# Optimization experiments

Measured on AMD Instinct MI355X. Metric: run time of the kernel, lower is better.

The kernel has to match this reference:

```python
import math
import jax, jax.numpy as jnp
import numpy as np

# ---- config (matches init_kwargs) ----
HIDDEN = 2048
N_HEADS = 16
Q_LORA = 1536
KV_LORA = 512
NOPE = 128
ROPE = 64
VHD = 128
QHD = NOPE + ROPE  # 192
BASE = 10000.0
SCALE = 40.0
ORIG_MAX = 4096
BETA_FAST = 32
BETA_SLOW = 1
MSCALE = 1.0
MSCALE_ALL = 1.0
EPS = 1e-6


def yarn_get_mscale(scale=1.0, mscale=1.0):
    if scale <= 1:
        return 1.0
    return 0.1 * mscale * math.log(scale) + 1.0


def yarn_cos_sin(seq_len):
    dim = ROPE
    ar = np.arange(0, dim, 2, dtype=np.float32)
    freq_extra = 1.0 / BASE ** (ar / dim)
    freq_inter = 1.0 / (SCALE * BASE ** (ar / dim))
    low = math.floor(dim * math.log(ORIG_MAX / (BETA_FAST * 2 * math.pi)) / (2 * math.log(BASE)))
    high = math.ceil(dim * math.log(ORIG_MAX / (BETA_SLOW * 2 * math.pi)) / (2 * math.log(BASE)))
    low, high = max(low, 0), min(high, dim - 1)
    denom = (high - low) if high != low else 0.001
    ramp = np.clip((np.arange(dim // 2, dtype=np.float32) - low) / denom, 0.0, 1.0)
    inv_freq_mask = 1.0 - ramp
    inv_freq = freq_inter * (1.0 - inv_freq_mask) + freq_extra * inv_freq_mask
    t = np.arange(seq_len, dtype=np.float32)
    freqs = np.outer(t, inv_freq)
    emb = np.concatenate([freqs, freqs], axis=-1)
    _m = yarn_get_mscale(SCALE, MSCALE) / yarn_get_mscale(SCALE, MSCALE_ALL)
    return jnp.asarray(np.cos(emb) * _m), jnp.asarray(np.sin(emb) * _m)


def rms_norm(x, w, eps=EPS):
    xf = x.astype(jnp.float32)
    var = jnp.mean(xf * xf, axis=-1, keepdims=True)
    return (w * (xf * jax.lax.rsqrt(var + eps)).astype(x.dtype))


def _rotate_half(x):
    x1, x2 = jnp.split(x, 2, axis=-1)
    return jnp.concatenate([-x2, x1], axis=-1)


def _interleave_to_half(x):
    # view(b,h,s,d//2,2).transpose(4,3).reshape(b,h,s,d)
    b, h, s, d = x.shape
    return jnp.swapaxes(x.reshape(b, h, s, d // 2, 2), -1, -2).reshape(b, h, s, d)


def apply_rope(q, k, cos, sin, position_ids):
    cos = cos[position_ids][:, None]  # [b,1,s,d]
    sin = sin[position_ids][:, None]
    q = _interleave_to_half(q)
    k = _interleave_to_half(k)
    q_emb = q * cos + _rotate_half(q) * sin
    k_emb = k * cos + _rotate_half(k) * sin
    return q_emb, k_emb


def mla_forward(hidden_states, position_ids, wq_a, q_a_ln_w, wq_b, wkv_a, kv_a_ln_w, wkv_b, wo):
    b, s, _ = hidden_states.shape
    # Q: low-rank down, RMSNorm, up
    q = rms_norm(hidden_states @ wq_a.T, q_a_ln_w) @ wq_b.T        # [b,s,H*QHD]
    q = q.reshape(b, s, N_HEADS, QHD).transpose(0, 2, 1, 3)        # [b,H,s,QHD]
    q_nope, q_pe = q[..., :NOPE], q[..., NOPE:]
    # KV: compressed latent + shared rope key
    ckv = hidden_states @ wkv_a.T                                   # [b,s,KV_LORA+ROPE]
    compressed, k_pe = ckv[..., :KV_LORA], ckv[..., KV_LORA:]
    k_pe = k_pe.reshape(b, s, 1, ROPE).transpose(0, 2, 1, 3)       # [b,1,s,ROPE]
    kv = rms_norm(compressed, kv_a_ln_w) @ wkv_b.T                  # [b,s,H*(NOPE+VHD)]
    kv = kv.reshape(b, s, N_HEADS, NOPE + VHD).transpose(0, 2, 1, 3)
    k_nope, value_states = kv[..., :NOPE], kv[..., NOPE:]
    # decoupled RoPE on rope dims only
    cos, sin = yarn_cos_sin(s)
    q_pe, k_pe = apply_rope(q_pe, k_pe, cos, sin, position_ids)
    query = jnp.concatenate([q_nope, q_pe], axis=-1)                # [b,H,s,QHD]
    key = jnp.concatenate(
        [k_nope, jnp.broadcast_to(k_pe, (b, N_HEADS, s, ROPE))], axis=-1)
    # softmax scale with YaRN mscale correction
    softmax_scale = QHD ** -0.5
    if MSCALE_ALL:
        m = yarn_get_mscale(SCALE, MSCALE_ALL)
        softmax_scale = softmax_scale * m * m
    attn = jnp.einsum('bhqd,bhkd->bhqk', query, key) * softmax_scale
    causal = jnp.tril(jnp.ones((s, s), dtype=bool))
    attn = jnp.where(causal, attn, jnp.finfo(attn.dtype).min)
    attn = jax.nn.softmax(attn.astype(jnp.float32), axis=-1).astype(query.dtype)
    out = jnp.einsum('bhqk,bhkd->bhqd', attn, value_states)         # [b,H,s,VHD]
    out = out.transpose(0, 2, 1, 3).reshape(b, s, N_HEADS * VHD)
    return out @ wo.T


def setup_inputs() -> dict:
    key = jax.random.key(0)
    ks = jax.random.split(key, 8)
    b, s = 2, 2048
    std = 0.02
    return {
        'hidden_states': jax.random.normal(ks[0], (b, s, HIDDEN), jnp.float32),
        'position_ids': jnp.broadcast_to(jnp.arange(s, dtype=jnp.int32), (b, s)),
        'wq_a': jax.random.normal(ks[1], (Q_LORA, HIDDEN), jnp.float32) * std,
        'q_a_ln_w': jnp.ones((Q_LORA,), jnp.float32),
        'wq_b': jax.random.normal(ks[2], (N_HEADS * QHD, Q_LORA), jnp.float32) * std,
        'wkv_a': jax.random.normal(ks[3], (KV_LORA + ROPE, HIDDEN), jnp.float32) * std,
        'kv_a_ln_w': jnp.ones((KV_LORA,), jnp.float32),
        'wkv_b': jax.random.normal(ks[4], (N_HEADS * (NOPE + VHD), KV_LORA), jnp.float32) * std,
        'wo': jax.random.normal(ks[5], (HIDDEN, N_HEADS * VHD), jnp.float32) * std,
    }


def reference(hidden_states, position_ids, wq_a, q_a_ln_w, wq_b, wkv_a, kv_a_ln_w, wkv_b, wo):
    return mla_forward(hidden_states, position_ids, wq_a, q_a_ln_w, wq_b,
                       wkv_a, kv_a_ln_w, wkv_b, wo)
```

## Files before the change

### kernel.cpp

```cpp
#include <hip/hip_runtime.h>
#include <hip/hip_bf16.h>
#include <math.h>

typedef __bf16 bf16_t;
typedef __bf16 bf16x4 __attribute__((ext_vector_type(4)));
typedef __bf16 bf16x8 __attribute__((ext_vector_type(8)));
typedef float floatx4 __attribute__((ext_vector_type(4)));

#define MFMA16(a, b, c) __builtin_amdgcn_mfma_f32_16x16x32_bf16((a), (b), (c), 0, 0, 0)

#define NEG_BIG (-1e30f)

__device__ __forceinline__ void gload16(const bf16_t* g, bf16_t* l) {
    __builtin_amdgcn_global_load_lds(
        (const __attribute__((address_space(1))) unsigned int*)g,
        (__attribute__((address_space(3))) unsigned int*)l,
        16, 0, 0);
}

__global__ void detect_kernel(const unsigned int* __restrict__ lnw, int* __restrict__ flag) {
    if (threadIdx.x == 0 && blockIdx.x == 0)
        flag[0] = (lnw[0] == 0x3F803F80u) ? 1 : 0;
}

__global__ __launch_bounds__(256) void conv_in_kernel(const void* __restrict__ src,
                                                      bf16_t* __restrict__ dst,
                                                      long nchunk,
                                                      const int* __restrict__ flag) {
    long i = (long)blockIdx.x * 256 + threadIdx.x;
    if (i >= nchunk) return;
    if (flag[0]) {
        ((uint4*)dst)[i] = ((const uint4*)src)[i];
    } else {
        const float* f = (const float*)src + i * 8;
        bf16x8 o;
#pragma unroll
        for (int j = 0; j < 8; ++j) o[j] = (bf16_t)f[j];
        ((bf16x8*)dst)[i] = o;
    }
}

__global__ __launch_bounds__(256) void conv_in_scale_kernel(const void* __restrict__ src,
                                                            bf16_t* __restrict__ dst,
                                                            long nchunk,
                                                            const int* __restrict__ flag,
                                                            float s) {
    long i = (long)blockIdx.x * 256 + threadIdx.x;
    if (i >= nchunk) return;
    bf16x8 o;
    if (flag[0]) {
        bf16x8 v = ((const bf16x8*)src)[i];
#pragma unroll
        for (int j = 0; j < 8; ++j) o[j] = (bf16_t)((float)v[j] * s);
    } else {
        const float* f = (const float*)src + i * 8;
#pragma unroll
        for (int j = 0; j < 8; ++j) o[j] = (bf16_t)(f[j] * s);
    }
    ((bf16x8*)dst)[i] = o;
}

__global__ __launch_bounds__(256) void conv_ln_kernel(const void* __restrict__ qsrc,
                                                      const void* __restrict__ kvsrc,
                                                      bf16_t* __restrict__ qd,
                                                      bf16_t* __restrict__ kvd,
                                                      const int* __restrict__ flag) {
    int t = threadIdx.x;
    const void* src = (t < 192) ? qsrc : kvsrc;
    bf16_t* dst = (t < 192) ? qd : kvd;
    int i = (t < 192) ? t : (t - 192);
    bf16x8 o;
    if (flag[0]) {
        o = ((const bf16x8*)src)[i];
    } else {
        const float* f = (const float*)src + i * 8;
#pragma unroll
        for (int j = 0; j < 8; ++j) o[j] = (bf16_t)f[j];
    }
    ((bf16x8*)dst)[i] = o;
}

__global__ __launch_bounds__(256) void pad_wkv_kernel(const void* __restrict__ src,
                                                      bf16_t* __restrict__ dst,
                                                      const int* __restrict__ flag) {
    long idx = (long)blockIdx.x * 256 + threadIdx.x;
    long e0 = idx * 8;
    if (e0 >= (long)640 * 2048) return;
    int row = (int)(e0 >> 11);
    bf16x8 v;
#pragma unroll
    for (int j = 0; j < 8; ++j) v[j] = (bf16_t)0.0f;
    if (row < 576) {
        if (flag[0]) {
            v = *(const bf16x8*)((const bf16_t*)src + e0);
        } else {
            const float* f = (const float*)src + e0;
#pragma unroll
            for (int j = 0; j < 8; ++j) v[j] = (bf16_t)f[j];
        }
    }
    *(bf16x8*)(dst + e0) = v;
}

#define GEMM_STAGE(bufsel) do { \
        gload16(Ag, &As[bufsel][(wave * 2 + 0) * 512]); \
        gload16(Ag + r16, &As[bufsel][(wave * 2 + 1) * 512]); \
        gload16(Bg, &Bs[bufsel][(wave * 2 + 0) * 512]); \
        gload16(Bg + r16, &Bs[bufsel][(wave * 2 + 1) * 512]); \
        Ag += 32; Bg += 32; } while (0)

#define GEMM_PIPELINE_BODY \
    int tid = threadIdx.x; \
    int lane = tid & 63; \
    int wave = tid >> 6; \
    int m0 = blockIdx.x * 128; \
    int n0 = blockIdx.y * 128; \
    int wm = (wave & 1) * 64; \
    int wn = (wave >> 1) * 64; \
    int col = lane & 15; \
    int g = lane >> 4; \
    floatx4 acc[4][4] = {}; \
    int srow = wave * 32 + (lane >> 2); \
    int scol = ((lane & 3) ^ (srow & 3)) * 8; \
    const bf16_t* Ag = A + (size_t)(m0 + srow) * K + scol; \
    const bf16_t* Bg = B + (size_t)(n0 + srow) * K + scol; \
    size_t r16 = (size_t)16 * K; \
    int rchunk = (g ^ (col & 3)) * 8; \
    int nk = K >> 5; \
    GEMM_STAGE(0); \
    GEMM_STAGE(1); \
    int cur = 0; \
    for (int kt = 0; kt < nk; ++kt) { \
        if (kt + 1 < nk) asm volatile("s_waitcnt vmcnt(4)" ::: "memory"); \
        else             asm volatile("s_waitcnt vmcnt(0)" ::: "memory"); \
        __builtin_amdgcn_s_barrier(); \
        __builtin_amdgcn_sched_barrier(0); \
        bf16x8 af[4], bfr[4]; \
        _Pragma("unroll") \
        for (int i = 0; i < 4; ++i) af[i] = *(const bf16x8*)(&As[cur][(wm + i * 16 + col) * 32 + rchunk]); \
        _Pragma("unroll") \
        for (int j = 0; j < 4; ++j) bfr[j] = *(const bf16x8*)(&Bs[cur][(wn + j * 16 + col) * 32 + rchunk]); \
        _Pragma("unroll") \
        for (int i = 0; i < 4; ++i) \
            _Pragma("unroll") \
            for (int j = 0; j < 4; ++j) \
                acc[i][j] = MFMA16(af[i], bfr[j], acc[i][j]); \
        __builtin_amdgcn_sched_barrier(0); \
        __builtin_amdgcn_s_barrier(); \
        if (kt + 2 < nk) { GEMM_STAGE(cur); } \
        cur ^= 1; \
    }

__global__ __launch_bounds__(256) void gemm_bf16(const bf16_t* __restrict__ A,
                                                 const bf16_t* __restrict__ B,
                                                 bf16_t* __restrict__ C,
                                                 int M, int N, int K) {
    __shared__ __align__(16) bf16_t As[2][128 * 32];
    __shared__ __align__(16) bf16_t Bs[2][128 * 32];
    GEMM_PIPELINE_BODY

#pragma unroll
    for (int i = 0; i < 4; ++i)
#pragma unroll
        for (int j = 0; j < 4; ++j) {
            size_t mrow = (size_t)(m0 + wm + i * 16 + g * 4);
            size_t ncol = (size_t)(n0 + wn + j * 16 + col);
            bf16_t* cp = C + mrow * N + ncol;
#pragma unroll
            for (int r = 0; r < 4; ++r) cp[(size_t)r * N] = (bf16_t)acc[i][j][r];
        }
}

__global__ __launch_bounds__(256) void gemm_out(const bf16_t* __restrict__ A,
                                                const bf16_t* __restrict__ B,
                                                void* __restrict__ Cv,
                                                int M, int N, int K,
                                                const int* __restrict__ flag) {
    __shared__ __align__(16) bf16_t As[2][128 * 32];
    __shared__ __align__(16) bf16_t Bs[2][128 * 32];
    GEMM_PIPELINE_BODY

    if (flag[0]) {
        bf16_t* C = (bf16_t*)Cv;
#pragma unroll
        for (int i = 0; i < 4; ++i)
#pragma unroll
            for (int j = 0; j < 4; ++j) {
                size_t mrow = (size_t)(m0 + wm + i * 16 + g * 4);
                size_t ncol = (size_t)(n0 + wn + j * 16 + col);
                bf16_t* cp = C + mrow * N + ncol;
#pragma unroll
                for (int r = 0; r < 4; ++r) cp[(size_t)r * N] = (bf16_t)acc[i][j][r];
            }
    } else {
        float* C = (float*)Cv;
#pragma unroll
        for (int i = 0; i < 4; ++i)
#pragma unroll
            for (int j = 0; j < 4; ++j) {
                size_t mrow = (size_t)(m0 + wm + i * 16 + g * 4);
                size_t ncol = (size_t)(n0 + wn + j * 16 + col);
                float* cp = C + mrow * N + ncol;
#pragma unroll
                for (int r = 0; r < 4; ++r) cp[(size_t)r * N] = acc[i][j][r];
            }
    }
}

__global__ __launch_bounds__(256) void gemm_kv(const bf16_t* __restrict__ A,
                                               const bf16_t* __restrict__ B,
                                               bf16_t* __restrict__ ktile,
                                               bf16_t* __restrict__ vtile,
                                               int K) {
    __shared__ __align__(16) bf16_t As[2][128 * 32];
    __shared__ __align__(16) bf16_t Bs[2][128 * 32];
    GEMM_PIPELINE_BODY

#pragma unroll
    for (int i = 0; i < 4; ++i)
#pragma unroll
        for (int j = 0; j < 4; ++j) {
            int mrow = m0 + wm + i * 16 + g * 4;
            int ncol = n0 + wn + j * 16 + col;
            int h = ncol >> 8;
            int within = ncol & 255;
            if (within < 128) {
#pragma unroll
                for (int r = 0; r < 4; ++r) {
                    int tok = mrow + r;
                    int bb = tok >> 11, sx = tok & 2047;
                    int ktt = sx >> 6, row = sx & 63;
                    size_t ridx = ((size_t)(bb * 16 + h) * 32 + ktt) * 64 + row;
                    ktile[ridx * 192 + ((within >> 3) ^ (row & 7)) * 8 + (within & 7)] =
                        (bf16_t)acc[i][j][r];
                }
            } else {
                int d = within - 128;
                int bb = mrow >> 11, sx = mrow & 2047;
                int ktt = sx >> 6, w64 = sx & 63;
                int mtk = w64 >> 4, gp = (w64 >> 2) & 3;
                int pos = (mtk >> 1) * 32 + gp * 8 + (mtk & 1) * 4;
                size_t off = (((size_t)(bb * 16 + h) * 32 + ktt) * 128 + d) * 64
                             + ((pos >> 3) ^ (d & 7)) * 8 + (pos & 7);
                bf16x4 pk;
#pragma unroll
                for (int r = 0; r < 4; ++r) pk[r] = (bf16_t)acc[i][j][r];
                *(bf16x4*)(vtile + off) = pk;
            }
        }
}

__global__ __launch_bounds__(256) void rmsnorm_kernel(const bf16_t* __restrict__ in, int in_stride,
                                                      const bf16_t* __restrict__ w,
                                                      bf16_t* __restrict__ out, int out_stride,
                                                      int C) {
    int row = blockIdx.x;
    int tid = threadIdx.x;
    const bf16_t* x = in + (size_t)row * in_stride;
    bool act = tid * 8 < C;
    float xs[8];
    float ss = 0.f;
    if (act) {
        bf16x8 v = *(const bf16x8*)(x + tid * 8);
#pragma unroll
        for (int j = 0; j < 8; ++j) {
            xs[j] = (float)v[j];
            ss += xs[j] * xs[j];
        }
    }
    for (int o = 32; o; o >>= 1) ss += __shfl_xor(ss, o, 64);
    __shared__ float red[4];
    if ((tid & 63) == 0) red[tid >> 6] = ss;
    __syncthreads();
    float tot = red[0] + red[1] + red[2] + red[3];
    float scale = rsqrtf(tot / (float)C + 1e-6f);
    if (act) {
        bf16x8 wv = *(const bf16x8*)(w + tid * 8);
        bf16x8 ov;
#pragma unroll
        for (int j = 0; j < 8; ++j) ov[j] = (bf16_t)((float)wv[j] * xs[j] * scale);
        *(bf16x8*)(out + (size_t)row * out_stride + tid * 8) = ov;
    }
}

__global__ __launch_bounds__(256) void rope_kernel(bf16_t* __restrict__ q,
                                                   const bf16_t* __restrict__ ckv,
                                                   bf16_t* __restrict__ ktile,
                                                   const int* __restrict__ pos_ids) {
    int tid = threadIdx.x;
    int lane = tid & 63;
    int gwave = (blockIdx.x * 256 + tid) >> 6;
    int unit = gwave * 2 + ((lane >> 5) & 1);
    int j = lane & 31;
    if (unit >= 4096 * 17) return;
    int t = unit / 17;
    int head = unit % 17;

    float fe = __expf(-(float)j * 0.28782313662425575f);
    float fi = fe * 0.025f;
    float ramp = fminf(fmaxf(((float)j - 10.0f) / 13.0f, 0.0f), 1.0f);
    float invf = fi * ramp + fe * (1.0f - ramp);
    float th = (float)pos_ids[t] * invf;
    float c = cosf(th);
    float s = sinf(th);

    if (head < 16) {
        bf16_t* base = q + (size_t)t * 3072 + head * 192 + 128;
        float e = (float)base[2 * j];
        float o = (float)base[2 * j + 1];
        base[j] = (bf16_t)(e * c - o * s);
        base[j + 32] = (bf16_t)(o * c + e * s);
    } else {
        const bf16_t* src = ckv + (size_t)t * 640 + 512;
        float e = (float)src[2 * j];
        float o = (float)src[2 * j + 1];
        bf16_t rb = (bf16_t)(e * c - o * s);
        bf16_t ob = (bf16_t)(o * c + e * s);
        int bb = t >> 11, sx = t & 2047;
        int ktt = sx >> 6, row = sx & 63;
        int o1 = ((16 + (j >> 3)) ^ (row & 7)) * 8 + (j & 7);
        int o2 = ((20 + (j >> 3)) ^ (row & 7)) * 8 + (j & 7);
        size_t rb0 = ((size_t)(bb * 16) * 32 + ktt) * 64 + row;
#pragma unroll
        for (int hh = 0; hh < 16; ++hh) {
            bf16_t* kr = ktile + (rb0 + (size_t)hh * 2048) * 192;
            kr[o1] = rb;
            kr[o2] = ob;
        }
    }
}

__global__ __launch_bounds__(512, 4) void attn_kernel(const bf16_t* __restrict__ q,
                                                      const bf16_t* __restrict__ ktile,
                                                      const bf16_t* __restrict__ vtile,
                                                      bf16_t* __restrict__ outp) {
    __shared__ __align__(16) bf16_t Ks[2][64 * 192];
    __shared__ __align__(16) bf16_t Vt[2][128 * 64];

    int tid = threadIdx.x;
    int lane = tid & 63;
    int wave = tid >> 6;
    int lid = blockIdx.x + blockIdx.y * 16;
    int c = lid & 7;
    int r = lid >> 3;
    int x = (r & 15) ^ ((r >> 5) & 1);
    int y = c * 4 + (r >> 4);
    int qt0 = x >> 1;
    int qt = (x & 1) ? (15 - qt0) : qt0;
    if (y >= 16) qt = 15 - qt;
    int b = y >> 4;
    int h = y & 15;
    int q0 = qt * 128;
    size_t tok0 = (size_t)b * 2048;
    int col = lane & 15;
    int g = lane >> 4;

    bf16x8 qf[6];
    {
        const bf16_t* qb = q + (tok0 + q0 + wave * 16 + col) * 3072 + h * 192 + g * 8;
#pragma unroll
        for (int ks = 0; ks < 6; ++ks)
            qf[ks] = *(const bf16x8*)(qb + ks * 32);
    }

    const bf16_t* ksrc = ktile + (size_t)y * 32 * 12288 + wave * 1536 + lane * 8;
    const bf16_t* vsrc = vtile + (size_t)y * 32 * 8192 + wave * 1024 + lane * 8;

#define ATTN_STAGE(KT, BUF) do { \
        const bf16_t* kp_ = ksrc + (size_t)(KT) * 12288; \
        bf16_t* kd_ = &Ks[BUF][wave * 1536]; \
        gload16(kp_, kd_); \
        gload16(kp_ + 512, kd_ + 512); \
        gload16(kp_ + 1024, kd_ + 1024); \
        const bf16_t* vp_ = vsrc + (size_t)(KT) * 8192; \
        bf16_t* vd_ = &Vt[BUF][wave * 1024]; \
        gload16(vp_, vd_); \
        gload16(vp_ + 512, vd_ + 512); \
    } while (0)

    float m_i = NEG_BIG;
    floatx4 lacc = {};
    floatx4 o_acc[8] = {};
    int xsw = col & 7;
    bf16x8 onesv;
#pragma unroll
    for (int i = 0; i < 8; ++i) onesv[i] = (bf16_t)1.0f;

    ATTN_STAGE(0, 0);

    int niter = (q0 + 128) >> 6;
    for (int kt = 0; kt < niter; ++kt) {
        int k0 = kt * 64;
        int cur = kt & 1;

        asm volatile("s_waitcnt vmcnt(0)" ::: "memory");
        __builtin_amdgcn_s_barrier();
        __builtin_amdgcn_sched_barrier(0);

        if (kt + 1 < niter) ATTN_STAGE(kt + 1, cur ^ 1);

        if (k0 > q0 + wave * 16 + 15) continue;

        floatx4 s_acc[4] = {};
#pragma unroll
        for (int ks = 0; ks < 6; ++ks) {
            bf16x8 ak[4];
#pragma unroll
            for (int mt = 0; mt < 4; ++mt)
                ak[mt] = *(const bf16x8*)(&Ks[cur][(mt * 16 + col) * 192 + ((4 * ks + g) ^ xsw) * 8]);
            __builtin_amdgcn_s_setprio(1);
#pragma unroll
            for (int mt = 0; mt < 4; ++mt)
                s_acc[mt] = MFMA16(ak[mt], qf[ks], s_acc[mt]);
            __builtin_amdgcn_s_setprio(0);
        }

        bf16x8 bp[2];
        {
            int qg = q0 + wave * 16 + col;
            float tm[4];
            if (k0 + 63 > q0 + wave * 16) {
#pragma unroll
                for (int mt = 0; mt < 4; ++mt) {
#pragma unroll
                    for (int r2 = 0; r2 < 4; ++r2) {
                        int key = k0 + mt * 16 + g * 4 + r2;
                        float s = (key <= qg) ? s_acc[mt][r2] : NEG_BIG;
                        s_acc[mt][r2] = s;
                    }
                    tm[mt] = fmaxf(fmaxf(s_acc[mt][0], s_acc[mt][1]),
                                   fmaxf(s_acc[mt][2], s_acc[mt][3]));
                }
            } else {
#pragma unroll
                for (int mt = 0; mt < 4; ++mt)
                    tm[mt] = fmaxf(fmaxf(s_acc[mt][0], s_acc[mt][1]),
                                   fmaxf(s_acc[mt][2], s_acc[mt][3]));
            }
            float mx = fmaxf(fmaxf(tm[0], tm[1]), fmaxf(tm[2], tm[3]));
            mx = fmaxf(mx, __shfl_xor(mx, 16, 64));
            mx = fmaxf(mx, __shfl_xor(mx, 32, 64));
            bool defer = __all(mx <= m_i + 8.0f);
            if (!defer) {
                float mnew = fmaxf(m_i, mx);
                float alpha = exp2f(m_i - mnew);
                m_i = mnew;
#pragma unroll
                for (int r2 = 0; r2 < 4; ++r2) lacc[r2] *= alpha;
#pragma unroll
                for (int mt = 0; mt < 8; ++mt)
#pragma unroll
                    for (int r2 = 0; r2 < 4; ++r2)
                        o_acc[mt][r2] *= alpha;
            }
#pragma unroll
            for (int kc = 0; kc < 2; ++kc) {
                bf16x8 t;
#pragma unroll
                for (int half = 0; half < 2; ++half)
#pragma unroll
                    for (int r2 = 0; r2 < 4; ++r2)
                        t[half * 4 + r2] = (bf16_t)exp2f(s_acc[kc * 2 + half][r2] - m_i);
                bp[kc] = t;
            }
        }

#pragma unroll
        for (int kc = 0; kc < 2; ++kc) {
            lacc = MFMA16(onesv, bp[kc], lacc);
#pragma unroll
            for (int mt = 0; mt < 8; ++mt) {
                bf16x8 av = *(const bf16x8*)(&Vt[cur][(mt * 16 + col) * 64 + ((4 * kc + g) ^ xsw) * 8]);
                __builtin_amdgcn_s_setprio(1);
                o_acc[mt] = MFMA16(av, bp[kc], o_acc[mt]);
                __builtin_amdgcn_s_setprio(0);
            }
        }
    }

    {
        float inv = 1.0f / lacc[0];
        size_t trow = tok0 + q0 + wave * 16 + col;
        bf16_t* op = outp + trow * 2048 + h * 128;
#pragma unroll
        for (int mt = 0; mt < 8; ++mt) {
            bf16x4 pk;
#pragma unroll
            for (int r2 = 0; r2 < 4; ++r2) pk[r2] = (bf16_t)(o_acc[mt][r2] * inv);
            *(bf16x4*)(op + mt * 16 + g * 4) = pk;
        }
    }
#undef ATTN_STAGE
}

extern "C" void kernel_launch(void* const* d_in, const int* in_sizes, int n_in,
                              void* d_out, int out_size, void* d_ws, size_t ws_size,
                              hipStream_t stream) {
    const void* hidden_raw = d_in[0];
    const int* pos = (const int*)d_in[1];
    const void* wq_a_raw = d_in[2];
    const void* q_ln_raw = d_in[3];
    const void* wq_b_raw = d_in[4];
    const void* wkv_a_raw = d_in[5];
    const void* kv_ln_raw = d_in[6];
    const void* wkv_b_raw = d_in[7];
    const void* wo_raw = d_in[8];

    char* ws = (char*)d_ws;
    int* flag = (int*)ws;          ws += 256;
    bf16_t* wkv_pad = (bf16_t*)ws; ws += (size_t)640 * 2048 * 2;
    bf16_t* q_a     = (bf16_t*)ws; ws += (size_t)4096 * 1536 * 2;
    bf16_t* qbuf    = (bf16_t*)ws; ws += (size_t)4096 * 3072 * 2;
    bf16_t* ckv     = (bf16_t*)ws; ws += (size_t)4096 * 640 * 2;
    bf16_t* kv_n    = (bf16_t*)ws; ws += (size_t)4096 * 512 * 2;
    bf16_t* ktile   = (bf16_t*)ws; ws += (size_t)32 * 32 * 64 * 192 * 2;
    bf16_t* vtile   = (bf16_t*)ws; ws += (size_t)32 * 32 * 128 * 64 * 2;
    bf16_t* attno   = (bf16_t*)ws; ws += (size_t)4096 * 2048 * 2;
    bf16_t* hb      = (bf16_t*)ws; ws += (size_t)4096 * 2048 * 2;
    bf16_t* wqab    = (bf16_t*)ws; ws += (size_t)1536 * 2048 * 2;
    bf16_t* wqbb    = (bf16_t*)ws; ws += (size_t)3072 * 1536 * 2;
    bf16_t* wkvbb   = (bf16_t*)ws; ws += (size_t)4096 * 512 * 2;
    bf16_t* wob     = (bf16_t*)ws; ws += (size_t)2048 * 2048 * 2;
    bf16_t* qlnb    = (bf16_t*)ws; ws += 4096;
    bf16_t* kvlnb   = (bf16_t*)ws; ws += 4096;

    detect_kernel<<<1, 64, 0, stream>>>((const unsigned int*)q_ln_raw, flag);

    double m = 0.1 * log(40.0) + 1.0;
    float scale = (float)((m * m) / sqrt(192.0) * 1.4426950408889634);

    conv_in_kernel<<<4096, 256, 0, stream>>>(hidden_raw, hb, (long)4096 * 2048 / 8, flag);
    conv_in_kernel<<<1536, 256, 0, stream>>>(wq_a_raw, wqab, (long)1536 * 2048 / 8, flag);
    conv_ln_kernel<<<1, 256, 0, stream>>>(q_ln_raw, kv_ln_raw, qlnb, kvlnb, flag);
    conv_in_scale_kernel<<<2304, 256, 0, stream>>>(wq_b_raw, wqbb, (long)3072 * 1536 / 8, flag, scale);
    conv_in_kernel<<<1024, 256, 0, stream>>>(wkv_b_raw, wkvbb, (long)4096 * 512 / 8, flag);
    conv_in_kernel<<<2048, 256, 0, stream>>>(wo_raw, wob, (long)2048 * 2048 / 8, flag);
    pad_wkv_kernel<<<640, 256, 0, stream>>>(wkv_a_raw, wkv_pad, flag);

    gemm_bf16<<<dim3(32, 12), 256, 0, stream>>>(hb, wqab, q_a, 4096, 1536, 2048);
    gemm_bf16<<<dim3(32, 5), 256, 0, stream>>>(hb, wkv_pad, ckv, 4096, 640, 2048);

    rmsnorm_kernel<<<4096, 256, 0, stream>>>(q_a, 1536, qlnb, q_a, 1536, 1536);
    rmsnorm_kernel<<<4096, 256, 0, stream>>>(ckv, 640, kvlnb, kv_n, 512, 512);

    gemm_bf16<<<dim3(32, 24), 256, 0, stream>>>(q_a, wqbb, qbuf, 4096, 3072, 1536);
    gemm_kv<<<dim3(32, 32), 256, 0, stream>>>(kv_n, wkvbb, ktile, vtile, 512);

    rope_kernel<<<8704, 256, 0, stream>>>(qbuf, ckv, ktile, pos);

    attn_kernel<<<dim3(16, 32), 512, 0, stream>>>(qbuf, ktile, vtile, attno);

    gemm_out<<<dim3(32, 16), 256, 0, stream>>>(attno, wob, d_out, 4096, 2048, 2048, flag);
}
```

Measured before the change: 456.5 us.

## Merge q_a and ckv projection GEMMs and rebalance causal attention work per block

Moves the wq_a bf16 buffer so it sits directly before the padded wkv_a buffer in the workspace. This lets a single GEMM launch over 1536+640 output columns write q_a and ckv from one combined weight matrix, replacing two launches and filling the tail better. The attention kernel also changes its block-to-query mapping: each wave in a block now takes a 16-row query strip spaced 256 rows apart, so every block mixes short and long causal rows and blocks do similar amounts of work. The cost is that K/V tiles are streamed for the longest row in the block, and waves whose rows end earlier sit idle for those iterations.

```diff
diff --git a/kernel.cpp b/kernel.cpp
--- a/kernel.cpp
+++ b/kernel.cpp
@@ -171,6 +171,40 @@
         }
 }
 
+__global__ __launch_bounds__(256) void gemm_qa_ckv(const bf16_t* __restrict__ A,
+                                                   const bf16_t* __restrict__ B,
+                                                   bf16_t* __restrict__ qa,
+                                                   bf16_t* __restrict__ ckv,
+                                                   int K) {
+    __shared__ __align__(16) bf16_t As[2][128 * 32];
+    __shared__ __align__(16) bf16_t Bs[2][128 * 32];
+    GEMM_PIPELINE_BODY
+
+    if (n0 < 1536) {
+#pragma unroll
+        for (int i = 0; i < 4; ++i)
+#pragma unroll
+            for (int j = 0; j < 4; ++j) {
+                size_t mrow = (size_t)(m0 + wm + i * 16 + g * 4);
+                size_t ncol = (size_t)(n0 + wn + j * 16 + col);
+                bf16_t* cp = qa + mrow * 1536 + ncol;
+#pragma unroll
+                for (int r = 0; r < 4; ++r) cp[(size_t)r * 1536] = (bf16_t)acc[i][j][r];
+            }
+    } else {
+#pragma unroll
+        for (int i = 0; i < 4; ++i)
+#pragma unroll
+            for (int j = 0; j < 4; ++j) {
+                size_t mrow = (size_t)(m0 + wm + i * 16 + g * 4);
+                size_t ncol = (size_t)(n0 - 1536 + wn + j * 16 + col);
+                bf16_t* cp = ckv + mrow * 640 + ncol;
+#pragma unroll
+                for (int r = 0; r < 4; ++r) cp[(size_t)r * 640] = (bf16_t)acc[i][j][r];
+            }
+    }
+}
+
 __global__ __launch_bounds__(256) void gemm_out(const bf16_t* __restrict__ A,
                                                 const bf16_t* __restrict__ B,
                                                 void* __restrict__ Cv,
@@ -343,21 +377,18 @@
     int lid = blockIdx.x + blockIdx.y * 16;
     int c = lid & 7;
     int r = lid >> 3;
-    int x = (r & 15) ^ ((r >> 5) & 1);
+    int qt = r & 15;
     int y = c * 4 + (r >> 4);
-    int qt0 = x >> 1;
-    int qt = (x & 1) ? (15 - qt0) : qt0;
-    if (y >= 16) qt = 15 - qt;
     int b = y >> 4;
     int h = y & 15;
-    int q0 = qt * 128;
     size_t tok0 = (size_t)b * 2048;
     int col = lane & 15;
     int g = lane >> 4;
+    int qrow = qt * 16 + wave * 256;
 
     bf16x8 qf[6];
     {
-        const bf16_t* qb = q + (tok0 + q0 + wave * 16 + col) * 3072 + h * 192 + g * 8;
+        const bf16_t* qb = q + (tok0 + qrow + col) * 3072 + h * 192 + g * 8;
 #pragma unroll
         for (int ks = 0; ks < 6; ++ks)
             qf[ks] = *(const bf16x8*)(qb + ks * 32);
@@ -388,7 +419,7 @@
 
     ATTN_STAGE(0, 0);
 
-    int niter = (q0 + 128) >> 6;
+    int niter = (qt * 16 + 1871) >> 6;
     for (int kt = 0; kt < niter; ++kt) {
         int k0 = kt * 64;
         int cur = kt & 1;
@@ -399,7 +430,7 @@
 
         if (kt + 1 < niter) ATTN_STAGE(kt + 1, cur ^ 1);
 
-        if (k0 > q0 + wave * 16 + 15) continue;
+        if (k0 > qrow + 15) continue;
 
         floatx4 s_acc[4] = {};
 #pragma unroll
@@ -417,9 +448,9 @@
 
         bf16x8 bp[2];
         {
-            int qg = q0 + wave * 16 + col;
+            int qg = qrow + col;
             float tm[4];
-            if (k0 + 63 > q0 + wave * 16) {
+            if (k0 + 63 > qrow) {
 #pragma unroll
                 for (int mt = 0; mt < 4; ++mt) {
 #pragma unroll
@@ -480,7 +511,7 @@
 
     {
         float inv = 1.0f / lacc[0];
-        size_t trow = tok0 + q0 + wave * 16 + col;
+        size_t trow = tok0 + qrow + col;
         bf16_t* op = outp + trow * 2048 + h * 128;
 #pragma unroll
         for (int mt = 0; mt < 8; ++mt) {
@@ -508,6 +539,7 @@
 
     char* ws = (char*)d_ws;
     int* flag = (int*)ws;          ws += 256;
+    bf16_t* wqab    = (bf16_t*)ws; ws += (size_t)1536 * 2048 * 2;
     bf16_t* wkv_pad = (bf16_t*)ws; ws += (size_t)640 * 2048 * 2;
     bf16_t* q_a     = (bf16_t*)ws; ws += (size_t)4096 * 1536 * 2;
     bf16_t* qbuf    = (bf16_t*)ws; ws += (size_t)4096 * 3072 * 2;
@@ -517,7 +549,6 @@
     bf16_t* vtile   = (bf16_t*)ws; ws += (size_t)32 * 32 * 128 * 64 * 2;
     bf16_t* attno   = (bf16_t*)ws; ws += (size_t)4096 * 2048 * 2;
     bf16_t* hb      = (bf16_t*)ws; ws += (size_t)4096 * 2048 * 2;
-    bf16_t* wqab    = (bf16_t*)ws; ws += (size_t)1536 * 2048 * 2;
     bf16_t* wqbb    = (bf16_t*)ws; ws += (size_t)3072 * 1536 * 2;
     bf16_t* wkvbb   = (bf16_t*)ws; ws += (size_t)4096 * 512 * 2;
     bf16_t* wob     = (bf16_t*)ws; ws += (size_t)2048 * 2048 * 2;
@@ -537,8 +568,7 @@
     conv_in_kernel<<<2048, 256, 0, stream>>>(wo_raw, wob, (long)2048 * 2048 / 8, flag);
     pad_wkv_kernel<<<640, 256, 0, stream>>>(wkv_a_raw, wkv_pad, flag);
 
-    gemm_bf16<<<dim3(32, 12), 256, 0, stream>>>(hb, wqab, q_a, 4096, 1536, 2048);
-    gemm_bf16<<<dim3(32, 5), 256, 0, stream>>>(hb, wkv_pad, ckv, 4096, 640, 2048);
+    gemm_qa_ckv<<<dim3(32, 17), 256, 0, stream>>>(hb, wqab, q_a, ckv, 2048);
 
     rmsnorm_kernel<<<4096, 256, 0, stream>>>(q_a, 1536, qlnb, q_a, 1536, 1536);
     rmsnorm_kernel<<<4096, 256, 0, stream>>>(ckv, 640, kvlnb, kv_n, 512, 512);
```

New measurement: 441.8 us. -3.2%, faster.
